# Kernel optimization log

Measured on AMD Instinct MI355X. Metric: run time of the kernel, lower is better.

The kernel has to match this reference:

```python
import jax, jax.numpy as jnp
import numpy as np

LORA_RANK = 16
LORA_ALPHA = 16
LORA_SCALE = LORA_ALPHA / LORA_RANK


def setup_inputs() -> dict:
    key = jax.random.key(0)
    k1, k2, k3, k4, k5 = jax.random.split(key, 5)
    B, S, D_IN, D_OUT, N_LORA, R = 8, 2048, 4096, 4096, 3, LORA_RANK
    std = 1.0 / np.sqrt(D_IN)
    x = jax.random.normal(k1, (B, S, D_IN), dtype=jnp.float32)
    weight = jax.random.truncated_normal(k2, -3.0, 3.0, (D_OUT, D_IN), dtype=jnp.float32) * std
    bias = jax.random.normal(k3, (D_OUT,), dtype=jnp.float32) * 0.01
    lora_A = jax.random.normal(k4, (N_LORA, R, D_IN), dtype=jnp.float32) * std
    lora_B = jax.random.normal(k5, (N_LORA, D_OUT, R), dtype=jnp.float32) * 0.02
    # segment starts: samples 0-1 -> no LoRA (index 0 reserved), 2-3 -> adapter 1, 4-5 -> adapter 2, 6-7 -> adapter 3
    lora_start_indices = jnp.arange(4, dtype=jnp.int64) * 2
    return {"x": x, "weight": weight, "bias": bias, "lora_A": lora_A,
            "lora_B": lora_B, "lora_start_indices": lora_start_indices}


def reference(x, weight, bias, lora_A, lora_B, lora_start_indices):
    # Base linear: y = x @ W^T + b   (torch: weight @ x_column)
    y = jnp.einsum('bsd,od->bso', x, weight) + bias  # [B,S,D_out]
    B = x.shape[0]
    # Map each batch sample to its segment (SGMV-style dispatch over contiguous segments).
    seg = jnp.searchsorted(lora_start_indices, jnp.arange(B), side='right') - 1  # [B], 0 = no LoRA
    adapter_idx = jnp.clip(seg - 1, 0, lora_A.shape[0] - 1)
    A = lora_A[adapter_idx]   # [B, r, D_in]  (tiny gather)
    Bw = lora_B[adapter_idx]  # [B, D_out, r]
    lo = jnp.einsum('bsr,bor->bso', jnp.einsum('bsd,brd->bsr', x, A), Bw) * LORA_SCALE
    use_lora = (seg > 0)[:, None, None]
    return y + jnp.where(use_lora, lo, jnp.zeros((), dtype=y.dtype))
```

## Files before the change

### kernel.cpp

```cpp
#include <hip/hip_runtime.h>


typedef __attribute__((ext_vector_type(8))) short short8;
typedef __attribute__((ext_vector_type(4))) float f32x4;
typedef __attribute__((ext_vector_type(4))) unsigned short u16x4;
typedef unsigned short u16;

typedef __attribute__((address_space(1))) void as1_void;
typedef __attribute__((address_space(3))) void as3_void;

#define M_DIM 16384
#define N_DIM 4096
#define K_DIM 4096
#define K2 8192
#define BM 256
#define BN 256
#define BK 64

__device__ __forceinline__ u16 f2bf(float f) {
  union { float f; unsigned u; } v; v.f = f;
  unsigned r = (v.u + 0x7FFFu + ((v.u >> 16) & 1u)) >> 16;
  return (u16)r;
}
__device__ __forceinline__ float bf2f(u16 u) {
  union { unsigned u; float f; } v; v.u = ((unsigned)u) << 16;
  return v.f;
}
__device__ __forceinline__ void gload16(const void* g, void* lds) {
  __builtin_amdgcn_global_load_lds((as1_void*)g, (as3_void*)lds, 16, 0, 0);
}
__device__ __forceinline__ int seg_of_batch(const int* starts, int b) {
  int seg = -1;
#pragma unroll
  for (int i = 0; i < 4; ++i) seg += (starts[i] <= b) ? 1 : 0;
  return seg;
}

#define VMCNT(n) asm volatile("s_waitcnt vmcnt(" #n ")" ::: "memory")
#define BAR() __builtin_amdgcn_s_barrier()

__global__ __launch_bounds__(256) void prep_kernel(
    const float* __restrict__ x, const float* __restrict__ wgt,
    const float* __restrict__ lA, const float* __restrict__ lB,
    u16* __restrict__ xbf, u16* __restrict__ wbf,
    u16* __restrict__ abf, u16* __restrict__ bw) {
  const long long NX4 = 16777216LL;
  const long long NW4 = 4194304LL;
  const long long NA4 = 49152LL;
  const long long NB  = 12288LL;
  const long long total = NX4 + NW4 + NA4 + NB;
  const f32x4* x4 = (const f32x4*)x;
  const f32x4* w4 = (const f32x4*)wgt;
  const f32x4* a4 = (const f32x4*)lA;
  u16x4* xo = (u16x4*)xbf;
  u16x4* wo = (u16x4*)wbf;
  u16x4* ao = (u16x4*)abf;
  for (long long i = (long long)blockIdx.x * blockDim.x + threadIdx.x; i < total;
       i += (long long)gridDim.x * blockDim.x) {
    if (i < NX4) {
      f32x4 v = x4[i];
      u16x4 o = {f2bf(v.x), f2bf(v.y), f2bf(v.z), f2bf(v.w)};
      xo[i] = o;
    } else if (i < NX4 + NW4) {
      long long j = i - NX4;
      f32x4 v = w4[j];
      u16x4 o = {f2bf(v.x), f2bf(v.y), f2bf(v.z), f2bf(v.w)};
      wo[j] = o;
    } else if (i < NX4 + NW4 + NA4) {
      long long j = i - NX4 - NW4;
      f32x4 v = a4[j];
      u16x4 o = {f2bf(v.x), f2bf(v.y), f2bf(v.z), f2bf(v.w)};
      ao[j] = o;
    } else {
      long long p = i - NX4 - NW4 - NA4;
      const float* src = lB + p * 16;
      u16* dst = bw + p * 32;
#pragma unroll
      for (int j = 0; j < 16; ++j) dst[j] = f2bf(src[j]);
#pragma unroll
      for (int j = 16; j < 32; ++j) dst[j] = 0;
    }
  }
}

__global__ __launch_bounds__(256) void ucompute_kernel(
    const u16* __restrict__ xbf, const u16* __restrict__ abf,
    const int* __restrict__ starts, u16* __restrict__ u) {
  const int l = threadIdx.x & 63;
  const int w = threadIdx.x >> 6;
  const int mbase = blockIdx.x * 16 + w * 4;
  const int b = mbase >> 11;
  const int seg = seg_of_batch(starts, b);
  const int use = seg > 0;
  int ad = seg - 1; ad = ad < 0 ? 0 : (ad > 2 ? 2 : ad);

  float acc[4][16];
#pragma unroll
  for (int row = 0; row < 4; ++row)
#pragma unroll
    for (int r = 0; r < 16; ++r) acc[row][r] = 0.f;

  if (use) {
    const u16* xr = xbf + (size_t)mbase * K_DIM + l * 8;
    const u16* ar = abf + (size_t)ad * (16 * K_DIM) + l * 8;
    for (int pass = 0; pass < 8; ++pass) {
      const int off = pass * 512;
      float xv[4][8];
#pragma unroll
      for (int row = 0; row < 4; ++row) {
        short8 xs = *(const short8*)(xr + (size_t)row * K_DIM + off);
#pragma unroll
        for (int j = 0; j < 8; ++j) xv[row][j] = bf2f((u16)xs[j]);
      }
#pragma unroll
      for (int r = 0; r < 16; ++r) {
        short8 av = *(const short8*)(ar + (size_t)r * K_DIM + off);
#pragma unroll
        for (int j = 0; j < 8; ++j) {
          float a = bf2f((u16)av[j]);
#pragma unroll
          for (int row = 0; row < 4; ++row) acc[row][r] += xv[row][j] * a;
        }
      }
    }
  }
#pragma unroll
  for (int row = 0; row < 4; ++row) {
    float myval = 0.f;
#pragma unroll
    for (int r = 0; r < 16; ++r) {
      float v = acc[row][r];
      v += __shfl_xor(v, 32);
      v += __shfl_xor(v, 16);
      v += __shfl_xor(v, 8);
      v += __shfl_xor(v, 4);
      v += __shfl_xor(v, 2);
      v += __shfl_xor(v, 1);
      if (l == r) myval = v;
    }
    if (l < 32) u[(size_t)(mbase + row) * 32 + l] = (l < 16) ? f2bf(myval) : (u16)0;
  }
}


#define STAGE_A(buf, ih, kt) do { \
  gload16(aSrc + (size_t)((ih)*64) * K2 + (size_t)(kt)*128, \
          &As[buf][((ih)*64) * BK] + w * 512); \
  gload16(aSrc + (size_t)((ih)*64 + 128) * K2 + (size_t)(kt)*128, \
          &As[buf][((ih)*64 + 128) * BK] + w * 512); \
} while (0)
#define STAGE_B(buf, jh, kt) do { \
  gload16(bSrc + (size_t)((jh)*32) * K2 + (size_t)(kt)*128, \
          &Bs[buf][((jh)*32 + (w >> 2)*64) * BK] + (w & 3) * 512); \
  gload16(bSrc + (size_t)((jh)*32 + 128) * K2 + (size_t)(kt)*128, \
          &Bs[buf][((jh)*32 + (w >> 2)*64 + 128) * BK] + (w & 3) * 512); \
} while (0)

#define READ_A(dst, buf, ih) do { \
  _Pragma("unroll") \
  for (int i2 = 0; i2 < 4; ++i2) { \
    const u16* ar = &As[buf][(wr*128 + (ih)*64 + i2*16 + fm) * BK]; \
    dst[i2][0] = *(const short8*)(ar + c0); \
    dst[i2][1] = *(const short8*)(ar + c1); \
  } \
} while (0)
#define READ_B(dst, buf, jh) do { \
  _Pragma("unroll") \
  for (int j2 = 0; j2 < 2; ++j2) { \
    const u16* br = &Bs[buf][(wc*64 + (jh)*32 + j2*16 + fm) * BK]; \
    dst[j2][0] = *(const short8*)(br + c0); \
    dst[j2][1] = *(const short8*)(br + c1); \
  } \
} while (0)

#define MFMA16(ih, jh, A, B) do { \
  __builtin_amdgcn_s_setprio(1); \
  _Pragma("unroll") \
  for (int i2 = 0; i2 < 4; ++i2) \
  _Pragma("unroll") \
  for (int j2 = 0; j2 < 2; ++j2) { \
    acc[(ih)*4 + i2][(jh)*2 + j2] = __builtin_amdgcn_mfma_f32_16x16x32_bf16( \
        A[i2][0], B[j2][0], acc[(ih)*4 + i2][(jh)*2 + j2], 0, 0, 0); \
    acc[(ih)*4 + i2][(jh)*2 + j2] = __builtin_amdgcn_mfma_f32_16x16x32_bf16( \
        A[i2][1], B[j2][1], acc[(ih)*4 + i2][(jh)*2 + j2], 0, 0, 0); \
  } \
  __builtin_amdgcn_s_setprio(0); \
} while (0)

__global__ __launch_bounds__(512, 2) void gemm8_kernel(
    const u16* __restrict__ xbf, const u16* __restrict__ wbf,
    const float* __restrict__ bias, const u16* __restrict__ ubuf,
    const u16* __restrict__ bwpad, const int* __restrict__ starts,
    float* __restrict__ out) {
  __shared__ u16 As[2][BM * BK];
  __shared__ u16 Bs[2][BN * BK];

  const int tid = threadIdx.x;
  const int l = tid & 63;
  const int w = tid >> 6;

  const int bid = blockIdx.x;
  const int nb = (bid & 7) * 128 + (bid >> 3);
  const int m0 = (nb >> 4) << 8;
  const int n0 = (nb & 15) << 8;

  const int b = m0 >> 11;
  const int seg = seg_of_batch(starts, b);
  int ad = seg - 1; ad = ad < 0 ? 0 : (ad > 2 ? 2 : ad);

  const int lrow = l >> 3;
  const int swzslot = (l & 7) ^ lrow;
  const char* aSrc = (const char*)xbf +
      (size_t)(m0 + 8 * w + lrow) * K2 + swzslot * 16;
  const char* bSrc = (const char*)wbf +
      (size_t)(n0 + (w >> 2) * 64 + (w & 3) * 8 + lrow) * K2 + swzslot * 16;

  const int fm = l & 15;
  const int q = l >> 4;
  const int wr = w >> 2;
  const int wc = w & 3;
  const int c0 = ((q ^ (fm & 7)) * 8);
  const int c1 = (((q + 4) ^ (fm & 7)) * 8);

  f32x4 acc[8][4];
  const f32x4 z4 = {0.f, 0.f, 0.f, 0.f};
#pragma unroll
  for (int i = 0; i < 8; ++i)
#pragma unroll
    for (int j = 0; j < 4; ++j) acc[i][j] = z4;

  short8 aF0r[4][2];
  short8 aF1r[4][2];
  short8 bF0A[2][2];
  short8 bF0B[2][2];
  short8 bF1r[2][2];

  STAGE_A(0, 0, 0); STAGE_B(0, 0, 0); STAGE_B(0, 1, 0); STAGE_A(0, 1, 0);
  STAGE_A(1, 0, 1); STAGE_B(1, 1, 1); STAGE_A(1, 1, 1);
  VMCNT(6);
  BAR();
  READ_A(aF0r, 0, 0);
  READ_B(bF0B, 0, 0);

  for (int s = 0; s < 32; ++s) {
    const int t1 = 2 * s + 1;
    const int t2 = 2 * s + 2;
    const int t3 = 2 * s + 3;
    const bool more = (s < 31);

    STAGE_B(1, 0, t1);
    BAR();
    READ_B(bF1r, 0, 1);
    MFMA16(0, 0, aF0r, bF0B);
    BAR();

    if (more) STAGE_A(0, 0, t2);
    BAR();
    READ_A(aF1r, 0, 1);
    MFMA16(0, 1, aF0r, bF1r);
    BAR();

    if (more) STAGE_B(0, 1, t2);
    BAR();
    MFMA16(1, 1, aF1r, bF1r);
    BAR();

    if (more) STAGE_A(0, 1, t2);
    if (more) { VMCNT(6); } else { VMCNT(0); }
    BAR();
    READ_A(aF0r, 1, 0);
    READ_B(bF0A, 1, 0);
    MFMA16(1, 0, aF1r, bF0B);
    BAR();

    if (more) STAGE_B(0, 0, t2);
    BAR();
    READ_B(bF1r, 1, 1);
    MFMA16(0, 0, aF0r, bF0A);
    BAR();

    if (more) STAGE_A(1, 0, t3);
    BAR();
    READ_A(aF1r, 1, 1);
    MFMA16(0, 1, aF0r, bF1r);
    BAR();

    if (more) STAGE_B(1, 1, t3);
    BAR();
    MFMA16(1, 1, aF1r, bF1r);
    BAR();

    if (more) STAGE_A(1, 1, t3);
    if (more) { VMCNT(6); } else { VMCNT(0); }
    BAR();
    if (more) {
      READ_A(aF0r, 0, 0);
      READ_B(bF0B, 0, 0);
    }
    MFMA16(1, 0, aF1r, bF0A);
    BAR();
  }

  {
    u16* la = &As[0][0];
    u16* lb = &Bs[0][0];
    const int ls = l & 3;
    const int lr = l >> 2;
    const char* uSrc = (const char*)ubuf +
        (size_t)(m0 + 16 * w + lr) * 64 + ls * 16;
    const char* vSrc = (const char*)bwpad +
        ((size_t)ad * N_DIM + n0 + 16 * w + lr) * 64 + ls * 16;
    gload16(uSrc, la + (16 * w) * 32);
    gload16(uSrc + (size_t)128 * 64, la + (128 + 16 * w) * 32);
    gload16(vSrc, lb + (16 * w) * 32);
    gload16(vSrc + (size_t)128 * 64, lb + (128 + 16 * w) * 32);
    VMCNT(0);
    BAR();
    short8 aF[8], bF[4];
#pragma unroll
    for (int i = 0; i < 8; ++i)
      aF[i] = *(const short8*)(la + (wr * 128 + i * 16 + fm) * 32 + q * 8);
#pragma unroll
    for (int j = 0; j < 4; ++j)
      bF[j] = *(const short8*)(lb + (wc * 64 + j * 16 + fm) * 32 + q * 8);
#pragma unroll
    for (int i = 0; i < 8; ++i)
#pragma unroll
      for (int j = 0; j < 4; ++j)
        acc[i][j] = __builtin_amdgcn_mfma_f32_16x16x32_bf16(aF[i], bF[j],
                                                            acc[i][j], 0, 0, 0);
  }

  float bv[4];
#pragma unroll
  for (int j = 0; j < 4; ++j) bv[j] = bias[n0 + wc * 64 + j * 16 + fm];
#pragma unroll
  for (int i = 0; i < 8; ++i) {
#pragma unroll
    for (int ii = 0; ii < 4; ++ii) {
      const int m = m0 + wr * 128 + i * 16 + q * 4 + ii;
      float* orow = out + (size_t)m * N_DIM + n0 + wc * 64 + fm;
#pragma unroll
      for (int j = 0; j < 4; ++j) orow[j * 16] = acc[i][j][ii] + bv[j];
    }
  }
}

__global__ __launch_bounds__(256) void u_f32_kernel(
    const float* __restrict__ x, const float* __restrict__ lA,
    const int* __restrict__ starts, float* __restrict__ u) {
  const int l = threadIdx.x & 63;
  const int w = threadIdx.x >> 6;
  const int m = blockIdx.x * 4 + w;
  const int b = m >> 11;
  const int seg = seg_of_batch(starts, b);
  const int use = seg > 0;
  int ad = seg - 1; ad = ad < 0 ? 0 : (ad > 2 ? 2 : ad);
  float acc[16];
#pragma unroll
  for (int r = 0; r < 16; ++r) acc[r] = 0.f;
  if (use) {
    const float* xr = x + (size_t)m * K_DIM + l * 4;
    const float* ar = lA + (size_t)ad * (16 * K_DIM) + l * 4;
    for (int pass = 0; pass < 16; ++pass) {
      const int off = pass * 256;
      f32x4 xv = *(const f32x4*)(xr + off);
#pragma unroll
      for (int r = 0; r < 16; ++r) {
        f32x4 av = *(const f32x4*)(ar + (size_t)r * K_DIM + off);
        acc[r] += xv.x * av.x + xv.y * av.y + xv.z * av.z + xv.w * av.w;
      }
    }
  }
  float myval = 0.f;
#pragma unroll
  for (int r = 0; r < 16; ++r) {
    float v = acc[r];
    v += __shfl_xor(v, 32);
    v += __shfl_xor(v, 16);
    v += __shfl_xor(v, 8);
    v += __shfl_xor(v, 4);
    v += __shfl_xor(v, 2);
    v += __shfl_xor(v, 1);
    if (l == r) myval = v;
  }
  if (l < 16) u[(size_t)m * 16 + l] = myval;
}

__global__ __launch_bounds__(256) void gemm_f32_fallback(
    const float* __restrict__ x, const float* __restrict__ wgt,
    const float* __restrict__ bias, const float* __restrict__ lB,
    const float* __restrict__ u, const int* __restrict__ starts,
    float* __restrict__ out) {
  __shared__ float xs[4096];
  const int m = blockIdx.y;
  const int n0 = blockIdx.x * 256;
  const int t = threadIdx.x;
  const f32x4* xr4 = (const f32x4*)(x + (size_t)m * K_DIM);
  f32x4* xs4 = (f32x4*)xs;
  for (int i = t; i < 1024; i += 256) xs4[i] = xr4[i];
  __syncthreads();
  const int b = m >> 11;
  const int seg = seg_of_batch(starts, b);
  const int use = seg > 0;
  int ad = seg - 1; ad = ad < 0 ? 0 : (ad > 2 ? 2 : ad);
  const int n = n0 + t;
  const f32x4* wr = (const f32x4*)(wgt + (size_t)n * K_DIM);
  float acc = 0.f;
  for (int kk = 0; kk < 1024; ++kk) {
    f32x4 wv = wr[kk];
    f32x4 xv = xs4[kk];
    acc += xv.x * wv.x + xv.y * wv.y + xv.z * wv.z + xv.w * wv.w;
  }
  acc += bias[n];
  if (use) {
    const float* Bn = lB + ((size_t)ad * N_DIM + n) * 16;
    const float* um = u + (size_t)m * 16;
    float lo = 0.f;
#pragma unroll
    for (int r = 0; r < 16; ++r) lo += um[r] * Bn[r];
    acc += lo;
  }
  out[(size_t)m * N_DIM + n] = acc;
}

extern "C" void kernel_launch(void* const* d_in, const int* in_sizes, int n_in,
                              void* d_out, int out_size, void* d_ws, size_t ws_size,
                              hipStream_t stream) {
  const float* x    = (const float*)d_in[0];
  const float* wgt  = (const float*)d_in[1];
  const float* bias = (const float*)d_in[2];
  const float* lA   = (const float*)d_in[3];
  const float* lB   = (const float*)d_in[4];
  const int* starts = (const int*)d_in[5];
  float* out = (float*)d_out;

  const size_t XBF_OFF = 0;
  const size_t WBF_OFF = 134217728;
  const size_t ABF_OFF = 167772160;
  const size_t BW_OFF  = 168165376;
  const size_t U_OFF   = 168951808;
  const size_t WS_NEEDED = 170000384;

  if (ws_size >= WS_NEEDED) {
    u16* xbf = (u16*)((char*)d_ws + XBF_OFF);
    u16* wbf = (u16*)((char*)d_ws + WBF_OFF);
    u16* abf = (u16*)((char*)d_ws + ABF_OFF);
    u16* bw  = (u16*)((char*)d_ws + BW_OFF);
    u16* u   = (u16*)((char*)d_ws + U_OFF);
    prep_kernel<<<8192, 256, 0, stream>>>(x, wgt, lA, lB, xbf, wbf, abf, bw);
    ucompute_kernel<<<1024, 256, 0, stream>>>(xbf, abf, starts, u);
    gemm8_kernel<<<1024, 512, 0, stream>>>(xbf, wbf, bias, u, bw, starts, out);
  } else {
    float* uf = (float*)d_ws;
    u_f32_kernel<<<4096, 256, 0, stream>>>(x, lA, starts, uf);
    gemm_f32_fallback<<<dim3(16, 16384), 256, 0, stream>>>(x, wgt, bias, lB, uf, starts, out);
  }
}
```

Measured before the change: 1.211 ms.

## Restructure GEMM main loop to interleave MFMA, LDS reads and staging per phase

Rewrites the software-pipelined main loop so that each of eight phases issues MFMAs, LDS fragment reads and global-to-LDS stage loads together between single barriers, instead of separating them with paired barriers. It shortens the prefetch lookahead: the prologue stages only tile 0 and waits for it fully, and each half-tile is staged within the same iteration rather than one tile ahead. It also merges the two B fragment register buffers into one. The intent is to cut barrier count and register pressure while overlapping compute with loads, at the risk of exposing more global memory latency through the shallower prefetch and the tighter VMCNT waits.

```diff
diff --git a/kernel.cpp b/kernel.cpp
--- a/kernel.cpp
+++ b/kernel.cpp
@@ -231,74 +231,65 @@
 
   short8 aF0r[4][2];
   short8 aF1r[4][2];
-  short8 bF0A[2][2];
-  short8 bF0B[2][2];
+  short8 bF0r[2][2];
   short8 bF1r[2][2];
 
   STAGE_A(0, 0, 0); STAGE_B(0, 0, 0); STAGE_B(0, 1, 0); STAGE_A(0, 1, 0);
-  STAGE_A(1, 0, 1); STAGE_B(1, 1, 1); STAGE_A(1, 1, 1);
-  VMCNT(6);
+  VMCNT(0);
   BAR();
   READ_A(aF0r, 0, 0);
-  READ_B(bF0B, 0, 0);
+  READ_B(bF0r, 0, 0);
 
   for (int s = 0; s < 32; ++s) {
     const int t1 = 2 * s + 1;
     const int t2 = 2 * s + 2;
-    const int t3 = 2 * s + 3;
     const bool more = (s < 31);
 
+    BAR();
+    MFMA16(0, 0, aF0r, bF0r);
+    READ_B(bF1r, 0, 1);
+    STAGE_A(1, 0, t1);
+    STAGE_B(1, 1, t1);
+    VMCNT(4);
+
+    BAR();
+    MFMA16(0, 1, aF0r, bF1r);
+    READ_A(aF1r, 0, 1);
     STAGE_B(1, 0, t1);
-    BAR();
-    READ_B(bF1r, 0, 1);
-    MFMA16(0, 0, aF0r, bF0B);
-    BAR();
-
+
+    BAR();
+    MFMA16(1, 1, aF1r, bF1r);
+    STAGE_A(1, 1, t1);
+    VMCNT(2);
+
+    BAR();
+    MFMA16(1, 0, aF1r, bF0r);
+    READ_A(aF0r, 1, 0);
+    READ_B(bF0r, 1, 0);
     if (more) STAGE_A(0, 0, t2);
-    BAR();
-    READ_A(aF1r, 0, 1);
+
+    BAR();
+    MFMA16(0, 0, aF0r, bF0r);
+    READ_B(bF1r, 1, 1);
+    if (more) STAGE_B(0, 1, t2);
+    if (more) { VMCNT(4); } else { VMCNT(0); }
+
+    BAR();
     MFMA16(0, 1, aF0r, bF1r);
-    BAR();
-
-    if (more) STAGE_B(0, 1, t2);
+    READ_A(aF1r, 1, 1);
+    if (more) STAGE_B(0, 0, t2);
+
     BAR();
     MFMA16(1, 1, aF1r, bF1r);
-    BAR();
-
     if (more) STAGE_A(0, 1, t2);
-    if (more) { VMCNT(6); } else { VMCNT(0); }
-    BAR();
-    READ_A(aF0r, 1, 0);
-    READ_B(bF0A, 1, 0);
-    MFMA16(1, 0, aF1r, bF0B);
-    BAR();
-
-    if (more) STAGE_B(0, 0, t2);
-    BAR();
-    READ_B(bF1r, 1, 1);
-    MFMA16(0, 0, aF0r, bF0A);
-    BAR();
-
-    if (more) STAGE_A(1, 0, t3);
-    BAR();
-    READ_A(aF1r, 1, 1);
-    MFMA16(0, 1, aF0r, bF1r);
-    BAR();
-
-    if (more) STAGE_B(1, 1, t3);
-    BAR();
-    MFMA16(1, 1, aF1r, bF1r);
-    BAR();
-
-    if (more) STAGE_A(1, 1, t3);
-    if (more) { VMCNT(6); } else { VMCNT(0); }
-    BAR();
+    if (more) { VMCNT(2); } else { VMCNT(0); }
+
+    BAR();
+    MFMA16(1, 0, aF1r, bF0r);
     if (more) {
       READ_A(aF0r, 0, 0);
-      READ_B(bF0B, 0, 0);
-    }
-    MFMA16(1, 0, aF1r, bF0A);
-    BAR();
+      READ_B(bF0r, 0, 0);
+    }
   }
 
   {
```

Result: faster. 1.098 ms (-9.3%).
